# Performance work log

Hardware: AMD Instinct MI355X
Metric: run time of the kernel (lower is better)

The kernel has to match this reference:

```python
import jax, jax.numpy as jnp
import numpy as np

NBINS = 100  # hard-coded in torch.histogram(first, 100)


def setup_inputs() -> dict:
    key = jax.random.key(0)
    k1, k2 = jax.random.split(key)
    z = jax.random.normal(k1, (100000, 16), dtype=jnp.float32)
    cluster_layer = jax.random.normal(k2, (16, 16), dtype=jnp.float32)
    return {"z": z, "cluster_layer": cluster_layer}


def _per_feature_hist(combined):
    """Equal-width per-feature histogram (torch.histogram(x, 100) semantics).
    combined: [N+C, F] -> edges [F, NBINS+1], counts [F, NBINS] (float)."""
    lo = combined.min(axis=0)          # [F]
    hi = combined.max(axis=0)          # [F]
    t = jnp.linspace(0.0, 1.0, NBINS + 1, dtype=combined.dtype)  # [NBINS+1]
    edges = lo[:, None] + (hi - lo)[:, None] * t[None, :]        # [F, NBINS+1]
    # bin assignment: left-closed bins, last bin right-closed (np/torch histogram)
    idx = jax.vmap(lambda e, v: jnp.searchsorted(e, v, side="right"),
                   in_axes=(0, 1))(edges, combined) - 1          # [F, N+C]
    idx = jnp.clip(idx, 0, NBINS - 1)
    counts = jax.vmap(lambda i: jnp.zeros((NBINS,), combined.dtype).at[i].add(1.0))(idx)
    return edges, counts


def _mass_dissimilarity(z, cluster_layer):
    N, F = z.shape
    C = cluster_layer.shape[0]
    combined = jax.lax.stop_gradient(jnp.concatenate([z, cluster_layer], axis=0))  # detach()
    edges, counts = _per_feature_hist(combined)          # [F,101], [F,100]

    # searchsorted(bins, .) - 1, per feature (side='left' like torch default)
    sample_bins = jax.vmap(lambda e, v: jnp.searchsorted(e, v, side="left"),
                           in_axes=(0, 1))(edges, z).T - 1              # [N, F]
    cluster_bins = jax.vmap(lambda e, v: jnp.searchsorted(e, v, side="left"),
                            in_axes=(0, 1))(edges, cluster_layer).T - 1  # [C, F]

    mx = jnp.maximum(sample_bins[:, None, :], cluster_bins[None, :, :])  # [N, C, F]
    mn = jnp.minimum(sample_bins[:, None, :], cluster_bins[None, :, :])  # [N, C, F]

    cum = jnp.cumsum(counts, axis=1)                     # [F, NBINS]
    f_idx = jnp.arange(F)                                # broadcasts over [N, C, F]
    is_zero = mn <= 0
    lo_idx = jnp.where(is_zero, 0, mn - 1)
    lo_sum = cum[f_idx, lo_idx]                          # [N, C, F]
    hi_sum = cum[f_idx, jnp.clip(mx, 0, NBINS - 1)]      # [N, C, F]
    sum_counts = jnp.where(is_zero, hi_sum, hi_sum - lo_sum)

    divisor = jnp.asarray(N + C, z.dtype)
    # len(counts)==1 in the original after reshape(1,1,F,NBINS), so no extra divide
    mass = jnp.sqrt(jnp.sum((sum_counts / divisor) ** 2, axis=2))  # [N, C]
    return mass


def reference(z, cluster_layer):
    # get_Q(z, 'mass'): q = 1/(1+mass), row-normalized
    q = 1.0 / (1.0 + _mass_dissimilarity(z, cluster_layer))
    q = q / jnp.sum(q, axis=1, keepdims=True)
    return q
```

## Files before the change

kernel.cpp:

```cpp
#include <hip/hip_runtime.h>
#include <stdint.h>

#define NBINS 100
#define FF 16
#define CC 16
#define MM_BLOCKS 256
#define MM_THREADS 1024
#define H_BLOCKS 256
#define H_THREADS 1024
#define SPB 64
#define M_THREADS 256


__device__ __forceinline__ unsigned enc_f(float v) {
    unsigned u = __float_as_uint(v);
    return (u & 0x80000000u) ? ~u : (u | 0x80000000u);
}
__device__ __forceinline__ float dec_f(unsigned e) {
    unsigned u = (e & 0x80000000u) ? (e ^ 0x80000000u) : ~e;
    return __uint_as_float(u);
}
__device__ __forceinline__ unsigned shfl_xor_u(unsigned x, int m) {
    return (unsigned)__shfl_xor((int)x, m, 64);
}
__device__ __forceinline__ float edgeval(float lo, float d, int k) {
    float tt = (k == NBINS) ? 1.0f : __fmul_rn((float)k, 0.01f);
    return __fadd_rn(lo, __fmul_rn(d, tt));
}
__device__ __forceinline__ int search_left(float v, float lo, float dd, float scl) {
    int ig = (int)((v - lo) * scl);
    int a = ig - 3;
    a = a < -1 ? -1 : (a > 95 ? 95 : a);
    int g = a;
#pragma unroll
    for (int j = 1; j <= 5; ++j) g += (edgeval(lo, dd, a + j) < v) ? 1 : 0;
    return g;
}
__device__ __forceinline__ int search_right(float v, float lo, float dd, float scl) {
    int ig = (int)((v - lo) * scl);
    int a = ig - 3;
    a = a < -1 ? -1 : (a > 95 ? 95 : a);
    int g = a;
#pragma unroll
    for (int j = 1; j <= 5; ++j) g += (edgeval(lo, dd, a + j) <= v) ? 1 : 0;
    return g;
}
__device__ __forceinline__ float qlook(const float* cumf, int g) {
    int i = g < 0 ? 0 : (g > NBINS - 1 ? NBINS - 1 : g);
    return cumf[i];
}
__device__ __forceinline__ float plook(const float* cumf, int g) {
    int i = g - 1;
    i = i > NBINS - 1 ? NBINS - 1 : i;
    return (g >= 1) ? cumf[i] : 0.0f;
}

__global__ __launch_bounds__(1024) void k_minmax(const float4* __restrict__ z4,
                                                 const float4* __restrict__ cl4,
                                                 int zn4, int total4,
                                                 unsigned* __restrict__ partials,
                                                 unsigned* __restrict__ counts) {
    int t = threadIdx.x;
    int gtid = blockIdx.x * MM_THREADS + t;
    if (gtid < FF * NBINS) counts[gtid] = 0u;

    unsigned mn[4] = {~0u, ~0u, ~0u, ~0u}, mx[4] = {0u, 0u, 0u, 0u};
    int stride = MM_BLOCKS * MM_THREADS;
    for (int i = gtid; i < total4; i += stride) {
        float4 v = (i < zn4) ? z4[i] : cl4[i - zn4];
        unsigned e;
        e = enc_f(v.x); mn[0] = min(mn[0], e); mx[0] = max(mx[0], e);
        e = enc_f(v.y); mn[1] = min(mn[1], e); mx[1] = max(mx[1], e);
        e = enc_f(v.z); mn[2] = min(mn[2], e); mx[2] = max(mx[2], e);
        e = enc_f(v.w); mn[3] = min(mn[3], e); mx[3] = max(mx[3], e);
    }
#pragma unroll
    for (int off = 4; off < 64; off <<= 1) {
#pragma unroll
        for (int c = 0; c < 4; ++c) {
            mn[c] = min(mn[c], shfl_xor_u(mn[c], off));
            mx[c] = max(mx[c], shfl_xor_u(mx[c], off));
        }
    }
    __shared__ unsigned smin[16][16], smax[16][16];
    int wave = t >> 6, lane = t & 63;
    if (lane < 4) {
#pragma unroll
        for (int c = 0; c < 4; ++c) {
            smin[wave][4 * lane + c] = mn[c];
            smax[wave][4 * lane + c] = mx[c];
        }
    }
    __syncthreads();
    if (t < 16) {
        unsigned um = ~0u, ux = 0u;
#pragma unroll
        for (int w = 0; w < 16; ++w) {
            um = min(um, smin[w][t]);
            ux = max(ux, smax[w][t]);
        }
        partials[blockIdx.x * 32 + t] = um;
        partials[blockIdx.x * 32 + 16 + t] = ux;
    }
}

__global__ __launch_bounds__(1024) void k_hist(const float4* __restrict__ z4,
                                               const float4* __restrict__ cl4,
                                               int zn4, int total4,
                                               const unsigned* __restrict__ partials,
                                               unsigned* __restrict__ counts,
                                               float* __restrict__ params) {
    __shared__ unsigned ulo[16], uhi[16];
    __shared__ float slo[16], sd[16], sscl[16];
    __shared__ unsigned sc[FF * NBINS];
    int t = threadIdx.x;
    for (int i = t; i < FF * NBINS; i += H_THREADS) sc[i] = 0u;
    if (t < 16) { ulo[t] = ~0u; uhi[t] = 0u; }
    __syncthreads();
    {
        int f = t & 15, b0 = (t >> 4) * (MM_BLOCKS / 64);
        unsigned um = ~0u, ux = 0u;
#pragma unroll
        for (int b = b0; b < b0 + MM_BLOCKS / 64; ++b) {
            um = min(um, partials[b * 32 + f]);
            ux = max(ux, partials[b * 32 + 16 + f]);
        }
        atomicMin(&ulo[f], um);
        atomicMax(&uhi[f], ux);
    }
    __syncthreads();
    if (t < 16) {
        float lo = dec_f(ulo[t]), hi = dec_f(uhi[t]);
        float d = __fsub_rn(hi, lo);
        slo[t] = lo; sd[t] = d;
        sscl[t] = d > 0.0f ? 100.0f / d : 0.0f;
        if (blockIdx.x == 0) {
            params[t] = lo; params[16 + t] = d; params[32 + t] = sscl[t];
        }
    }
    __syncthreads();

    int gtid = blockIdx.x * H_THREADS + t;
    int stride = H_BLOCKS * H_THREADS;
    int fb = (4 * gtid) & 15;
    float lo_c[4], d_c[4], scl_c[4];
#pragma unroll
    for (int c = 0; c < 4; ++c) {
        int f = (fb + c) & 15;
        lo_c[c] = slo[f]; d_c[c] = sd[f]; scl_c[c] = sscl[f];
    }
    for (int i = gtid; i < total4; i += stride) {
        float4 v4 = (i < zn4) ? z4[i] : cl4[i - zn4];
        float vv[4] = {v4.x, v4.y, v4.z, v4.w};
#pragma unroll
        for (int c = 0; c < 4; ++c) {
            int f = (fb + c) & 15;
            int g = search_right(vv[c], lo_c[c], d_c[c], scl_c[c]);
            g = g < 0 ? 0 : (g > NBINS - 1 ? NBINS - 1 : g);
            atomicAdd(&sc[f * NBINS + g], 1u);
        }
    }
    __syncthreads();
    for (int i = t; i < FF * NBINS; i += H_THREADS) {
        unsigned c = sc[i];
        if (c) atomicAdd(&counts[i], c);
    }
}

__global__ __launch_bounds__(256) void k_main(const float* __restrict__ z, int N,
                                              float inv_div,
                                              const unsigned* __restrict__ counts,
                                              const float* __restrict__ params,
                                              const float* __restrict__ cl,
                                              float* __restrict__ out) {
    __shared__ float sparam[48];
    __shared__ unsigned sc[FF * NBINS];
    __shared__ float scum[FF * NBINS];
    __shared__ float2 sqs[SPB * 17];
    __shared__ float2 sqp[FF * CC];
    int t = threadIdx.x;
    for (int i = t; i < FF * NBINS; i += M_THREADS) sc[i] = counts[i];
    if (t < 48) sparam[t] = params[t];
    __syncthreads();
    if (t < 16) {
        float s = 0.0f;
        const unsigned* cp = &sc[t * NBINS];
        float* fp = &scum[t * NBINS];
#pragma unroll
        for (int k = 0; k < NBINS; ++k) { s += (float)cp[k]; fp[k] = s; }
    }
    __syncthreads();
    {
        int c = t & 15, f = t >> 4;
        float v = cl[c * FF + f];
        int g = search_left(v, sparam[f], sparam[16 + f], sparam[32 + f]);
        const float* cumf = &scum[f * NBINS];
        sqp[f * CC + c] = make_float2(qlook(cumf, g), plook(cumf, g));
    }
    int n0 = blockIdx.x * SPB;
#pragma unroll
    for (int ns = 0; ns < SPB / 16; ++ns) {
        int nl = ns * 16 + (t >> 4), f = t & 15;
        int n = n0 + nl;
        if (n < N) {
            float v = z[(size_t)n * FF + f];
            int g = search_left(v, sparam[f], sparam[16 + f], sparam[32 + f]);
            const float* cumf = &scum[f * NBINS];
            sqs[nl * 17 + f] = make_float2(qlook(cumf, g), plook(cumf, g));
        }
    }
    __syncthreads();

#pragma unroll
    for (int ns = 0; ns < SPB / 16; ++ns) {
        int nl = ns * 16 + (t >> 4), c = t & 15;
        int n = n0 + nl;
        if (n < N) {
            float acc = 0.0f;
#pragma unroll
            for (int f = 0; f < FF; ++f) {
                float2 s = sqs[nl * 17 + f];
                float2 p = sqp[f * CC + c];
                float h = fmaxf(s.x, p.x);
                float l = fminf(s.y, p.y);
                float d = h - l;
                acc = fmaf(d, d, acc);
            }
            float mass = sqrtf(acc) * inv_div;
            float qq = 1.0f / (1.0f + mass);
            float rs = qq;
            rs += __shfl_xor(rs, 1, 64);
            rs += __shfl_xor(rs, 2, 64);
            rs += __shfl_xor(rs, 4, 64);
            rs += __shfl_xor(rs, 8, 64);
            out[(size_t)n * CC + c] = qq / rs;
        }
    }
}

extern "C" void kernel_launch(void* const* d_in, const int* in_sizes, int n_in,
                              void* d_out, int out_size, void* d_ws, size_t ws_size,
                              hipStream_t stream) {
    const float* z  = (const float*)d_in[0];
    const float* cl = (const float*)d_in[1];
    float* out = (float*)d_out;
    int N = in_sizes[0] / FF;

    char* ws = (char*)d_ws;
    unsigned* partials = (unsigned*)(ws);
    unsigned* counts   = (unsigned*)(ws + 32768);
    float*    params   = (float*)(ws + 39168);

    const float4* z4  = (const float4*)d_in[0];
    const float4* cl4 = (const float4*)d_in[1];
    int zn4 = N * FF / 4;
    int total4 = (N + CC) * FF / 4;
    float inv_div = 1.0f / (float)(N + CC);

    k_minmax<<<MM_BLOCKS, MM_THREADS, 0, stream>>>(z4, cl4, zn4, total4,
                                                   partials, counts);
    k_hist<<<H_BLOCKS, H_THREADS, 0, stream>>>(z4, cl4, zn4, total4,
                                               partials, counts, params);
    int mblocks = (N + SPB - 1) / SPB;
    k_main<<<mblocks, M_THREADS, 0, stream>>>(z, N, inv_div, counts, params,
                                              cl, out);
}
```

Before: 90.05 us.

## Fuse histogram and main kernels with a grid-wide atomic barrier

Merges the histogram kernel and the per-sample mass kernel into one persistent kernel of 256 blocks of 1024 threads. Blocks meet at a global atomic barrier after pushing their histogram counts, then loop over 64-row tiles of z to compute the output. This removes one kernel launch and the params round-trip through global memory. In exchange it relies on all 256 blocks being co-resident, and the main phase now runs with fewer, larger blocks that synchronise every round.

```diff
diff --git a/kernel.cpp b/kernel.cpp
--- a/kernel.cpp
+++ b/kernel.cpp
@@ -4,12 +4,10 @@
 #define NBINS 100
 #define FF 16
 #define CC 16
-#define MM_BLOCKS 256
+#define GRID 256
 #define MM_THREADS 1024
-#define H_BLOCKS 256
-#define H_THREADS 1024
-#define SPB 64
-#define M_THREADS 256
+#define K2_THREADS 1024
+#define SPR 64
 
 
 __device__ __forceinline__ unsigned enc_f(float v) {
@@ -59,13 +57,15 @@
                                                  const float4* __restrict__ cl4,
                                                  int zn4, int total4,
                                                  unsigned* __restrict__ partials,
-                                                 unsigned* __restrict__ counts) {
+                                                 unsigned* __restrict__ counts,
+                                                 unsigned* __restrict__ bar) {
     int t = threadIdx.x;
     int gtid = blockIdx.x * MM_THREADS + t;
     if (gtid < FF * NBINS) counts[gtid] = 0u;
+    if (gtid == FF * NBINS) *bar = 0u;
 
     unsigned mn[4] = {~0u, ~0u, ~0u, ~0u}, mx[4] = {0u, 0u, 0u, 0u};
-    int stride = MM_BLOCKS * MM_THREADS;
+    int stride = GRID * MM_THREADS;
     for (int i = gtid; i < total4; i += stride) {
         float4 v = (i < zn4) ? z4[i] : cl4[i - zn4];
         unsigned e;
@@ -104,24 +104,31 @@
     }
 }
 
-__global__ __launch_bounds__(1024) void k_hist(const float4* __restrict__ z4,
-                                               const float4* __restrict__ cl4,
-                                               int zn4, int total4,
-                                               const unsigned* __restrict__ partials,
-                                               unsigned* __restrict__ counts,
-                                               float* __restrict__ params) {
+__global__ __launch_bounds__(1024) void k_rest(
+        const float4* __restrict__ z4, const float4* __restrict__ cl4,
+        int zn4, int total4, int N, float inv_div,
+        const unsigned* __restrict__ partials, unsigned* __restrict__ counts,
+        unsigned* __restrict__ bar, const float* __restrict__ cl,
+        const float* __restrict__ z, float* __restrict__ out)
+{
     __shared__ unsigned ulo[16], uhi[16];
     __shared__ float slo[16], sd[16], sscl[16];
     __shared__ unsigned sc[FF * NBINS];
+    __shared__ float scum[FF * NBINS];
+    __shared__ float2 sqs[SPR * 17];
+    __shared__ float2 sqp[FF * CC];
     int t = threadIdx.x;
-    for (int i = t; i < FF * NBINS; i += H_THREADS) sc[i] = 0u;
+    int gtid = blockIdx.x * K2_THREADS + t;
+    int gsz = GRID * K2_THREADS;
+
+    for (int i = t; i < FF * NBINS; i += K2_THREADS) sc[i] = 0u;
     if (t < 16) { ulo[t] = ~0u; uhi[t] = 0u; }
     __syncthreads();
     {
-        int f = t & 15, b0 = (t >> 4) * (MM_BLOCKS / 64);
+        int f = t & 15, b0 = (t >> 4) * (GRID / 64);
         unsigned um = ~0u, ux = 0u;
 #pragma unroll
-        for (int b = b0; b < b0 + MM_BLOCKS / 64; ++b) {
+        for (int b = b0; b < b0 + GRID / 64; ++b) {
             um = min(um, partials[b * 32 + f]);
             ux = max(ux, partials[b * 32 + 16 + f]);
         }
@@ -134,14 +141,9 @@
         float d = __fsub_rn(hi, lo);
         slo[t] = lo; sd[t] = d;
         sscl[t] = d > 0.0f ? 100.0f / d : 0.0f;
-        if (blockIdx.x == 0) {
-            params[t] = lo; params[16 + t] = d; params[32 + t] = sscl[t];
-        }
-    }
-    __syncthreads();
-
-    int gtid = blockIdx.x * H_THREADS + t;
-    int stride = H_BLOCKS * H_THREADS;
+    }
+    __syncthreads();
+
     int fb = (4 * gtid) & 15;
     float lo_c[4], d_c[4], scl_c[4];
 #pragma unroll
@@ -149,7 +151,7 @@
         int f = (fb + c) & 15;
         lo_c[c] = slo[f]; d_c[c] = sd[f]; scl_c[c] = sscl[f];
     }
-    for (int i = gtid; i < total4; i += stride) {
+    for (int i = gtid; i < total4; i += gsz) {
         float4 v4 = (i < zn4) ? z4[i] : cl4[i - zn4];
         float vv[4] = {v4.x, v4.y, v4.z, v4.w};
 #pragma unroll
@@ -161,26 +163,24 @@
         }
     }
     __syncthreads();
-    for (int i = t; i < FF * NBINS; i += H_THREADS) {
+    for (int i = t; i < FF * NBINS; i += K2_THREADS) {
         unsigned c = sc[i];
         if (c) atomicAdd(&counts[i], c);
     }
-}
-
-__global__ __launch_bounds__(256) void k_main(const float* __restrict__ z, int N,
-                                              float inv_div,
-                                              const unsigned* __restrict__ counts,
-                                              const float* __restrict__ params,
-                                              const float* __restrict__ cl,
-                                              float* __restrict__ out) {
-    __shared__ float sparam[48];
-    __shared__ unsigned sc[FF * NBINS];
-    __shared__ float scum[FF * NBINS];
-    __shared__ float2 sqs[SPB * 17];
-    __shared__ float2 sqp[FF * CC];
-    int t = threadIdx.x;
-    for (int i = t; i < FF * NBINS; i += M_THREADS) sc[i] = counts[i];
-    if (t < 48) sparam[t] = params[t];
+    __syncthreads();
+
+    if (t == 0) {
+        __hip_atomic_fetch_add(bar, 1u, __ATOMIC_RELEASE, __HIP_MEMORY_SCOPE_AGENT);
+        while (__hip_atomic_load(bar, __ATOMIC_ACQUIRE, __HIP_MEMORY_SCOPE_AGENT)
+               < (unsigned)GRID) {
+            __builtin_amdgcn_s_sleep(2);
+        }
+    }
+    __syncthreads();
+
+    for (int i = t; i < FF * NBINS; i += K2_THREADS)
+        sc[i] = __hip_atomic_load(&counts[i], __ATOMIC_RELAXED,
+                                  __HIP_MEMORY_SCOPE_AGENT);
     __syncthreads();
     if (t < 16) {
         float s = 0.0f;
@@ -190,51 +190,54 @@
         for (int k = 0; k < NBINS; ++k) { s += (float)cp[k]; fp[k] = s; }
     }
     __syncthreads();
-    {
+    if (t < CC * FF) {
         int c = t & 15, f = t >> 4;
         float v = cl[c * FF + f];
-        int g = search_left(v, sparam[f], sparam[16 + f], sparam[32 + f]);
+        int g = search_left(v, slo[f], sd[f], sscl[f]);
         const float* cumf = &scum[f * NBINS];
         sqp[f * CC + c] = make_float2(qlook(cumf, g), plook(cumf, g));
     }
-    int n0 = blockIdx.x * SPB;
-#pragma unroll
-    for (int ns = 0; ns < SPB / 16; ++ns) {
-        int nl = ns * 16 + (t >> 4), f = t & 15;
-        int n = n0 + nl;
-        if (n < N) {
-            float v = z[(size_t)n * FF + f];
-            int g = search_left(v, sparam[f], sparam[16 + f], sparam[32 + f]);
-            const float* cumf = &scum[f * NBINS];
-            sqs[nl * 17 + f] = make_float2(qlook(cumf, g), plook(cumf, g));
-        }
-    }
-    __syncthreads();
-
-#pragma unroll
-    for (int ns = 0; ns < SPB / 16; ++ns) {
-        int nl = ns * 16 + (t >> 4), c = t & 15;
-        int n = n0 + nl;
-        if (n < N) {
-            float acc = 0.0f;
-#pragma unroll
-            for (int f = 0; f < FF; ++f) {
-                float2 s = sqs[nl * 17 + f];
-                float2 p = sqp[f * CC + c];
-                float h = fmaxf(s.x, p.x);
-                float l = fminf(s.y, p.y);
-                float d = h - l;
-                acc = fmaf(d, d, acc);
+    __syncthreads();
+
+    int nrounds = (N + SPR - 1) / SPR;
+    for (int r = blockIdx.x; r < nrounds; r += GRID) {
+        int n0 = r * SPR;
+        {
+            int nl = t >> 4, f = t & 15;
+            int n = n0 + nl;
+            if (n < N) {
+                float v = z[(size_t)n * FF + f];
+                int g = search_left(v, slo[f], sd[f], sscl[f]);
+                const float* cumf = &scum[f * NBINS];
+                sqs[nl * 17 + f] = make_float2(qlook(cumf, g), plook(cumf, g));
             }
-            float mass = sqrtf(acc) * inv_div;
-            float qq = 1.0f / (1.0f + mass);
-            float rs = qq;
-            rs += __shfl_xor(rs, 1, 64);
-            rs += __shfl_xor(rs, 2, 64);
-            rs += __shfl_xor(rs, 4, 64);
-            rs += __shfl_xor(rs, 8, 64);
-            out[(size_t)n * CC + c] = qq / rs;
-        }
+        }
+        __syncthreads();
+        {
+            int nl = t >> 4, c = t & 15;
+            int n = n0 + nl;
+            if (n < N) {
+                float acc = 0.0f;
+#pragma unroll
+                for (int f = 0; f < FF; ++f) {
+                    float2 s = sqs[nl * 17 + f];
+                    float2 p = sqp[f * CC + c];
+                    float h = fmaxf(s.x, p.x);
+                    float l = fminf(s.y, p.y);
+                    float d = h - l;
+                    acc = fmaf(d, d, acc);
+                }
+                float mass = sqrtf(acc) * inv_div;
+                float qq = 1.0f / (1.0f + mass);
+                float rs = qq;
+                rs += __shfl_xor(rs, 1, 64);
+                rs += __shfl_xor(rs, 2, 64);
+                rs += __shfl_xor(rs, 4, 64);
+                rs += __shfl_xor(rs, 8, 64);
+                out[(size_t)n * CC + c] = qq / rs;
+            }
+        }
+        __syncthreads();
     }
 }
 
@@ -249,7 +252,7 @@
     char* ws = (char*)d_ws;
     unsigned* partials = (unsigned*)(ws);
     unsigned* counts   = (unsigned*)(ws + 32768);
-    float*    params   = (float*)(ws + 39168);
+    unsigned* bar      = (unsigned*)(ws + 39168);
 
     const float4* z4  = (const float4*)d_in[0];
     const float4* cl4 = (const float4*)d_in[1];
@@ -257,11 +260,8 @@
     int total4 = (N + CC) * FF / 4;
     float inv_div = 1.0f / (float)(N + CC);
 
-    k_minmax<<<MM_BLOCKS, MM_THREADS, 0, stream>>>(z4, cl4, zn4, total4,
-                                                   partials, counts);
-    k_hist<<<H_BLOCKS, H_THREADS, 0, stream>>>(z4, cl4, zn4, total4,
-                                               partials, counts, params);
-    int mblocks = (N + SPB - 1) / SPB;
-    k_main<<<mblocks, M_THREADS, 0, stream>>>(z, N, inv_div, counts, params,
-                                              cl, out);
-}
+    k_minmax<<<GRID, MM_THREADS, 0, stream>>>(z4, cl4, zn4, total4,
+                                              partials, counts, bar);
+    k_rest<<<GRID, K2_THREADS, 0, stream>>>(z4, cl4, zn4, total4, N, inv_div,
+                                            partials, counts, bar, cl, z, out);
+}
```

Measured after the change: 96.43 us. +7.1%, slower.

## Map one sample per thread in main kernel and parallelize cumsum scan

Applied to the files above, without the earlier changes.

Restructures k_main so each thread handles one full sample row: it loads 16 features with float4 loads, computes its bin lookups in registers, evaluates all 16 clusters and row-normalizes locally, then writes with float4 stores. This removes the shared-memory staging of per-sample lookups, the shuffle-based row sum and one barrier, and it cuts the per-block prologue cost by having 4x more samples per block (fewer blocks). The per-feature cumulative sum also changes from 16 serial threads to a 256-thread segmented shuffle scan. In exchange, register pressure rises and the strided per-thread row loads are less coalesced.

```diff
diff --git a/kernel.cpp b/kernel.cpp
--- a/kernel.cpp
+++ b/kernel.cpp
@@ -8,7 +8,6 @@
 #define MM_THREADS 1024
 #define H_BLOCKS 256
 #define H_THREADS 1024
-#define SPB 64
 #define M_THREADS 256
 
 
@@ -167,27 +166,44 @@
     }
 }
 
-__global__ __launch_bounds__(256) void k_main(const float* __restrict__ z, int N,
+__global__ __launch_bounds__(256) void k_main(const float4* __restrict__ z4, int N,
                                               float inv_div,
                                               const unsigned* __restrict__ counts,
                                               const float* __restrict__ params,
                                               const float* __restrict__ cl,
                                               float* __restrict__ out) {
     __shared__ float sparam[48];
-    __shared__ unsigned sc[FF * NBINS];
+    __shared__ float scnt[FF * NBINS];
     __shared__ float scum[FF * NBINS];
-    __shared__ float2 sqs[SPB * 17];
-    __shared__ float2 sqp[FF * CC];
+    __shared__ float sqp[CC * 32];
     int t = threadIdx.x;
-    for (int i = t; i < FF * NBINS; i += M_THREADS) sc[i] = counts[i];
     if (t < 48) sparam[t] = params[t];
-    __syncthreads();
-    if (t < 16) {
+    for (int i = t; i < FF * NBINS; i += M_THREADS) scnt[i] = (float)counts[i];
+    __syncthreads();
+    {
+        int f = t >> 4, j = t & 15;
+        int b0 = j * 7;
+        float loc[7];
         float s = 0.0f;
-        const unsigned* cp = &sc[t * NBINS];
-        float* fp = &scum[t * NBINS];
-#pragma unroll
-        for (int k = 0; k < NBINS; ++k) { s += (float)cp[k]; fp[k] = s; }
+#pragma unroll
+        for (int k = 0; k < 7; ++k) {
+            int b = b0 + k;
+            float v = (b < NBINS) ? scnt[f * NBINS + b] : 0.0f;
+            s += v;
+            loc[k] = s;
+        }
+        float ss = s;
+#pragma unroll
+        for (int off = 1; off < 16; off <<= 1) {
+            float up = __shfl_up(ss, off, 16);
+            if (j >= off) ss += up;
+        }
+        float pre = ss - s;
+#pragma unroll
+        for (int k = 0; k < 7; ++k) {
+            int b = b0 + k;
+            if (b < NBINS) scum[f * NBINS + b] = pre + loc[k];
+        }
     }
     __syncthreads();
     {
@@ -195,53 +211,70 @@
         float v = cl[c * FF + f];
         int g = search_left(v, sparam[f], sparam[16 + f], sparam[32 + f]);
         const float* cumf = &scum[f * NBINS];
-        sqp[f * CC + c] = make_float2(qlook(cumf, g), plook(cumf, g));
-    }
-    int n0 = blockIdx.x * SPB;
-#pragma unroll
-    for (int ns = 0; ns < SPB / 16; ++ns) {
-        int nl = ns * 16 + (t >> 4), f = t & 15;
-        int n = n0 + nl;
-        if (n < N) {
-            float v = z[(size_t)n * FF + f];
-            int g = search_left(v, sparam[f], sparam[16 + f], sparam[32 + f]);
-            const float* cumf = &scum[f * NBINS];
-            sqs[nl * 17 + f] = make_float2(qlook(cumf, g), plook(cumf, g));
-        }
-    }
-    __syncthreads();
-
-#pragma unroll
-    for (int ns = 0; ns < SPB / 16; ++ns) {
-        int nl = ns * 16 + (t >> 4), c = t & 15;
-        int n = n0 + nl;
-        if (n < N) {
-            float acc = 0.0f;
-#pragma unroll
-            for (int f = 0; f < FF; ++f) {
-                float2 s = sqs[nl * 17 + f];
-                float2 p = sqp[f * CC + c];
-                float h = fmaxf(s.x, p.x);
-                float l = fminf(s.y, p.y);
-                float d = h - l;
-                acc = fmaf(d, d, acc);
-            }
-            float mass = sqrtf(acc) * inv_div;
-            float qq = 1.0f / (1.0f + mass);
-            float rs = qq;
-            rs += __shfl_xor(rs, 1, 64);
-            rs += __shfl_xor(rs, 2, 64);
-            rs += __shfl_xor(rs, 4, 64);
-            rs += __shfl_xor(rs, 8, 64);
-            out[(size_t)n * CC + c] = qq / rs;
-        }
-    }
+        sqp[c * 32 + 2 * f]     = qlook(cumf, g);
+        sqp[c * 32 + 2 * f + 1] = plook(cumf, g);
+    }
+    __syncthreads();
+
+    int n = blockIdx.x * M_THREADS + t;
+    if (n >= N) return;
+
+    float v[FF];
+    const float4* zr = z4 + (size_t)n * 4;
+    float4 a0 = zr[0], a1 = zr[1], a2 = zr[2], a3 = zr[3];
+    v[0] = a0.x; v[1] = a0.y; v[2]  = a0.z; v[3]  = a0.w;
+    v[4] = a1.x; v[5] = a1.y; v[6]  = a1.z; v[7]  = a1.w;
+    v[8] = a2.x; v[9] = a2.y; v[10] = a2.z; v[11] = a2.w;
+    v[12] = a3.x; v[13] = a3.y; v[14] = a3.z; v[15] = a3.w;
+
+    float Qs[FF], Ps[FF];
+#pragma unroll
+    for (int f = 0; f < FF; ++f) {
+        int g = search_left(v[f], sparam[f], sparam[16 + f], sparam[32 + f]);
+        const float* cumf = &scum[f * NBINS];
+        Qs[f] = qlook(cumf, g);
+        Ps[f] = plook(cumf, g);
+    }
+
+    float q[CC];
+    float rowsum = 0.0f;
+#pragma unroll
+    for (int c = 0; c < CC; ++c) {
+        float acc = 0.0f;
+        const float4* qprow = (const float4*)&sqp[c * 32];
+#pragma unroll
+        for (int f2 = 0; f2 < 8; ++f2) {
+            float4 qp = qprow[f2];
+            float h0 = fmaxf(Qs[2 * f2], qp.x);
+            float l0 = fminf(Ps[2 * f2], qp.y);
+            float d0 = h0 - l0;
+            acc = fmaf(d0, d0, acc);
+            float h1 = fmaxf(Qs[2 * f2 + 1], qp.z);
+            float l1 = fminf(Ps[2 * f2 + 1], qp.w);
+            float d1 = h1 - l1;
+            acc = fmaf(d1, d1, acc);
+        }
+        float mass = sqrtf(acc) * inv_div;
+        float qq = 1.0f / (1.0f + mass);
+        q[c] = qq;
+        rowsum += qq;
+    }
+
+    float* op = out + (size_t)n * CC;
+    float4 o;
+    o.x = q[0] / rowsum;  o.y = q[1] / rowsum;  o.z = q[2] / rowsum;  o.w = q[3] / rowsum;
+    ((float4*)op)[0] = o;
+    o.x = q[4] / rowsum;  o.y = q[5] / rowsum;  o.z = q[6] / rowsum;  o.w = q[7] / rowsum;
+    ((float4*)op)[1] = o;
+    o.x = q[8] / rowsum;  o.y = q[9] / rowsum;  o.z = q[10] / rowsum; o.w = q[11] / rowsum;
+    ((float4*)op)[2] = o;
+    o.x = q[12] / rowsum; o.y = q[13] / rowsum; o.z = q[14] / rowsum; o.w = q[15] / rowsum;
+    ((float4*)op)[3] = o;
 }
 
 extern "C" void kernel_launch(void* const* d_in, const int* in_sizes, int n_in,
                               void* d_out, int out_size, void* d_ws, size_t ws_size,
                               hipStream_t stream) {
-    const float* z  = (const float*)d_in[0];
     const float* cl = (const float*)d_in[1];
     float* out = (float*)d_out;
     int N = in_sizes[0] / FF;
@@ -261,7 +294,7 @@
                                                    partials, counts);
     k_hist<<<H_BLOCKS, H_THREADS, 0, stream>>>(z4, cl4, zn4, total4,
                                                partials, counts, params);
-    int mblocks = (N + SPB - 1) / SPB;
-    k_main<<<mblocks, M_THREADS, 0, stream>>>(z, N, inv_div, counts, params,
+    int mblocks = (N + M_THREADS - 1) / M_THREADS;
+    k_main<<<mblocks, M_THREADS, 0, stream>>>(z4, N, inv_div, counts, params,
                                               cl, out);
 }
```

Measured after the change: 86.19 us (median of 2 runs). 1.04x faster.
